# Optimization experiments

Hardware: AMD Instinct MI355X
Metric: run time of the kernel (lower is better)

## Reference

```python
import jax, jax.numpy as jnp
import numpy as np

EPS = 1e-5

def layer_norm(x, g, b):
    mu = jnp.mean(x, axis=-1, keepdims=True)
    var = jnp.var(x, axis=-1, keepdims=True)
    return (x - mu) * jax.lax.rsqrt(var + EPS) * g + b

def setup_inputs() -> dict:
    key = jax.random.key(0)
    N, C, K = 50000, 64, 16
    ks = jax.random.split(key, 16)
    def lin(k, fan_in, fan_out):
        bound = 1.0 / np.sqrt(fan_in)
        kw, kb = jax.random.split(k)
        W = jax.random.uniform(kw, (fan_in, fan_out), minval=-bound, maxval=bound, dtype=jnp.float32)
        b = jax.random.uniform(kb, (fan_out,), minval=-bound, maxval=bound, dtype=jnp.float32)
        return W, b
    wq, bq = lin(ks[0], C, C)
    wk, bk = lin(ks[1], C, C)
    wv, bv = lin(ks[2], C, C)
    wp, bp = lin(ks[3], 3, C)
    wg1, bg1 = lin(ks[4], C, C)
    wg2, bg2 = lin(ks[5], C, C)
    wo, bo = lin(ks[6], C, C)
    return {
        'points': jax.random.normal(ks[7], (N, 3), dtype=jnp.float32),
        'features': jax.random.normal(ks[8], (N, C), dtype=jnp.float32),
        'neighbor_idx': jax.random.randint(ks[9], (N, K), 0, N, dtype=jnp.int32),
        'wq': wq, 'bq': bq, 'wk': wk, 'bk': bk, 'wv': wv, 'bv': bv,
        'wp': wp, 'bp': bp, 'gp': jnp.ones((C,), jnp.float32), 'betap': jnp.zeros((C,), jnp.float32),
        'wg1': wg1, 'bg1': bg1, 'gg': jnp.ones((C,), jnp.float32), 'betag': jnp.zeros((C,), jnp.float32),
        'wg2': wg2, 'bg2': bg2, 'wo': wo, 'bo': bo,
    }

def reference(points, features, neighbor_idx, wq, bq, wk, bk, wv, bv,
              wp, bp, gp, betap, wg1, bg1, gg, betag, wg2, bg2, wo, bo):
    # residual_proj is Identity since in_planes == out_planes
    residual = features
    q = features @ wq + bq                      # (N, C)
    k = features @ wk + bk
    v = features @ wv + bv
    gpts = points[neighbor_idx]                 # (N, K, 3)
    gk = k[neighbor_idx]                        # (N, K, C)
    gv = v[neighbor_idx]
    rel = gpts - points[:, None, :]             # (N, K, 3)
    p = jax.nn.relu(layer_norm(rel @ wp + bp, gp, betap))  # (N, K, C)
    attn_in = q[:, None, :] - gk + p            # (N, K, C)
    h = jax.nn.relu(layer_norm(attn_in @ wg1 + bg1, gg, betag))
    w = h @ wg2 + bg2                           # (N, K, C)
    w = jax.nn.softmax(w, axis=1)               # softmax over neighbor axis
    out = jnp.sum((gv + p) * w, axis=1)         # (N, C)
    return out @ wo + bo + residual
```

## Files before the change

### kernel.cpp

```cpp
#include <hip/hip_runtime.h>

typedef __attribute__((ext_vector_type(8))) short bfrag8;
typedef __attribute__((ext_vector_type(4))) short bfrag4;
typedef __attribute__((ext_vector_type(4))) float f32x4;

__device__ __forceinline__ float bf2f(unsigned short h){
  unsigned u = ((unsigned)h) << 16;
  return __builtin_bit_cast(float, u);
}
__device__ __forceinline__ unsigned short f2bf(float f){
  unsigned u = __builtin_bit_cast(unsigned, f);
  u = u + 0x7FFFu + ((u >> 16) & 1u);
  return (unsigned short)(u >> 16);
}
__device__ __forceinline__ bfrag8 gload8(const unsigned short* p){
  int4 v = *(const int4*)p;
  return __builtin_bit_cast(bfrag8, v);
}
__device__ __forceinline__ bfrag8 lds_load8(const unsigned short* p){
  bfrag4 lo = *(const bfrag4*)p;
  bfrag4 hi = *(const bfrag4*)(p + 4);
  bfrag8 r;
#pragma unroll
  for (int j = 0; j < 4; j++){ r[j] = lo[j]; r[4+j] = hi[j]; }
  return r;
}
__device__ __forceinline__ f32x4 mfma16(bfrag8 a, bfrag8 b, f32x4 c){
  return __builtin_amdgcn_mfma_f32_16x16x32_bf16(a, b, c, 0, 0, 0);
}

__device__ __forceinline__ float ldf(const void* p, size_t i, int f32){
  return f32 ? ((const float*)p)[i] : bf2f(((const unsigned short*)p)[i]);
}
__device__ __forceinline__ unsigned short ldbf(const void* p, size_t i, int f32){
  return f32 ? f2bf(((const float*)p)[i]) : ((const unsigned short*)p)[i];
}
__device__ __forceinline__ bfrag8 load8bf(const void* p, size_t base, int f32){
  if (f32){
    const float* f = (const float*)p + base;
    float4 x = *(const float4*)f;
    float4 y = *(const float4*)(f + 4);
    bfrag8 r;
    r[0]=(short)f2bf(x.x); r[1]=(short)f2bf(x.y); r[2]=(short)f2bf(x.z); r[3]=(short)f2bf(x.w);
    r[4]=(short)f2bf(y.x); r[5]=(short)f2bf(y.y); r[6]=(short)f2bf(y.z); r[7]=(short)f2bf(y.w);
    return r;
  }
  return gload8((const unsigned short*)p + base);
}

template<int CTRL>
__device__ __forceinline__ float dpp_add(float x){
  int xi = __builtin_bit_cast(int, x);
  int yi = __builtin_amdgcn_update_dpp(0, xi, CTRL, 0xF, 0xF, true);
  return x + __builtin_bit_cast(float, yi);
}
__device__ __forceinline__ float row16_sum(float x){
  x = dpp_add<0xB1>(x);
  x = dpp_add<0x4E>(x);
  x = dpp_add<0x141>(x);
  x = dpp_add<0x140>(x);
  return x;
}
__device__ __forceinline__ float xgrp_sum(float x){
  x += __shfl_xor(x, 16, 64);
  x += __shfl_xor(x, 32, 64);
  return x;
}
__device__ __forceinline__ float xgrp_max(float x){
  x = fmaxf(x, __shfl_xor(x, 16, 64));
  x = fmaxf(x, __shfl_xor(x, 32, 64));
  return x;
}
__device__ __forceinline__ int wave_isum(int x){
#pragma unroll
  for (int s = 1; s < 64; s <<= 1) x += __shfl_xor(x, s, 64);
  return x;
}

struct Ptrs { const void* p[21]; int n[21]; };
struct PrepPtrs { const void* w[6]; const void* wp; const void* b[11]; };

__global__ void detect_kernel(Ptrs ptrs, int* flags){
  const int lane = threadIdx.x & 63;
  const int wid = blockIdx.x * 4 + (threadIdx.x >> 6);
  if (wid >= 21) return;
  if (wid == 2){ if (lane == 0) flags[2] = 0; return; }

  const unsigned short* p = (const unsigned short*)ptrs.p[wid];
  int m = ptrs.n[wid]; if (m > 128) m = 128;
  int insane = 0, evenZero = 0, evenCnt = 0, oddNZ = 0, oddCnt = 0;
#pragma unroll
  for (int s = 0; s < 2; s++){
    int i = lane + s*64;
    if (i < m){
      unsigned short h = p[i];
      int e = (h >> 7) & 0xFF;
      bool z = (h & 0x7FFF) == 0;
      if (!z && (e == 0xFF || e < 90 || e > 140)) insane++;
      if (i & 1){ oddCnt++;  if (!z) oddNZ++; }
      else      { evenCnt++; if (z)  evenZero++; }
    }
  }
  insane = wave_isum(insane);
  evenZero = wave_isum(evenZero); evenCnt = wave_isum(evenCnt);
  oddNZ = wave_isum(oddNZ);       oddCnt = wave_isum(oddCnt);
  if (lane == 0){
    int f = 0;
    if (insane > 0) f = 1;
    else if (evenZero * 4 >= evenCnt * 3 && oddNZ * 4 >= oddCnt * 3) f = 1;
    flags[wid] = f;
  }
}

__global__ void prep_kernel(PrepPtrs pp, const int* __restrict__ flags,
                            unsigned short* __restrict__ wfrag,
                            unsigned short* __restrict__ wp_bf,
                            float* __restrict__ biases)
{
  const int gid = blockIdx.x * 256 + threadIdx.x;
  const int gstride = gridDim.x * 256;
  const int wflag[6] = {3,5,7,13,17,19};
  for (int idx = gid; idx < 6*4096; idx += gstride){
    int m = idx >> 12;
    int r = idx & 4095;
    int j = r & 7;
    int lane = (r >> 3) & 63;
    int kt = r >> 9;
    int ks = kt >> 2, t = kt & 3;
    int o = lane >> 4, rl = lane & 15;
    int src = (ks*32 + o*8 + j)*64 + t*16 + rl;
    wfrag[idx] = ldbf(pp.w[m], src, flags[wflag[m]]);
  }
  if (blockIdx.x == 0){
    for (int i = threadIdx.x; i < 192; i += 256) wp_bf[i] = ldbf(pp.wp, i, flags[9]);
    const int bflag[11] = {4,6,8,10,11,12,14,15,16,18,20};
    for (int i = threadIdx.x; i < 11*64; i += 256){
      int m = i >> 6;
      biases[i] = ldf(pp.b[m], i & 63, flags[bflag[m]]);
    }
  }
}

__global__ __launch_bounds__(256, 2)
void qkv_kernel(const void* __restrict__ feat,
                const unsigned short* __restrict__ wfrag,
                const float* __restrict__ biases,
                unsigned short* __restrict__ q_ws, unsigned short* __restrict__ k_ws,
                unsigned short* __restrict__ v_ws, const int* __restrict__ flags, int N)
{
  const int F_feat = flags[1];
  const int lane = threadIdx.x & 63;
  const int wave = threadIdx.x >> 6;
  const int o = lane >> 4, rl = lane & 15;

  bfrag8 wqf[2][4], wkf[2][4], wvf[2][4];
#pragma unroll
  for (int ks = 0; ks < 2; ks++)
#pragma unroll
    for (int t = 0; t < 4; t++){
      int off = ((ks*4 + t)*64 + lane)*8;
      wqf[ks][t] = gload8(wfrag + off);
      wkf[ks][t] = gload8(wfrag + 4096 + off);
      wvf[ks][t] = gload8(wfrag + 8192 + off);
    }
  float bqC[4], bkC[4], bvC[4];
#pragma unroll
  for (int t = 0; t < 4; t++){
    bqC[t] = biases[0*64 + t*16 + rl];
    bkC[t] = biases[1*64 + t*16 + rl];
    bvC[t] = biases[2*64 + t*16 + rl];
  }

  const int ntiles = (N + 15) >> 4;
  for (int tile = blockIdx.x*4 + wave; tile < ntiles; tile += gridDim.x*4){
    const int n0 = tile * 16;
    int ar = n0 + rl; if (ar >= N) ar = N - 1;
    bfrag8 a[2];
#pragma unroll
    for (int ks = 0; ks < 2; ks++) a[ks] = load8bf(feat, (size_t)ar*64 + ks*32 + o*8, F_feat);

#pragma unroll
    for (int t = 0; t < 4; t++){
      f32x4 zq = {0.f,0.f,0.f,0.f}, zk = {0.f,0.f,0.f,0.f}, zv = {0.f,0.f,0.f,0.f};
#pragma unroll
      for (int ks = 0; ks < 2; ks++){
        zq = mfma16(a[ks], wqf[ks][t], zq);
        zk = mfma16(a[ks], wkf[ks][t], zk);
        zv = mfma16(a[ks], wvf[ks][t], zv);
      }
#pragma unroll
      for (int q = 0; q < 4; q++){
        size_t row = n0 + o*4 + q; int col = t*16 + rl;
        if ((int)row < N){
          q_ws[row*64 + col] = f2bf(zq[q] + bqC[t]);
          k_ws[row*64 + col] = f2bf(zk[q] + bkC[t]);
          v_ws[row*64 + col] = f2bf(zv[q] + bvC[t]);
        }
      }
    }
  }
}

__global__ __launch_bounds__(256, 2)
void pt_kernel(const void* __restrict__ points,
               const void* __restrict__ feat,
               const int* __restrict__ nidx,
               const unsigned short* __restrict__ q_ws,
               const unsigned short* __restrict__ k_ws,
               const unsigned short* __restrict__ v_ws,
               const unsigned short* __restrict__ wfrag,
               const unsigned short* __restrict__ wp_bf,
               const float* __restrict__ biases,
               const int* __restrict__ flags, void* __restrict__ out, int N)
{
  __shared__ unsigned short xbuf[4][16][68];
  __shared__ unsigned short ybuf[4][64];

  const int F_pts = flags[0], F_feat = flags[1];
  const int lane = threadIdx.x & 63;
  const int wave = threadIdx.x >> 6;
  const int o = lane >> 4, rl = lane & 15;

  bfrag8 wg1f[2][4], wg2f[2][4], wof[2][4];
#pragma unroll
  for (int ks = 0; ks < 2; ks++)
#pragma unroll
    for (int t = 0; t < 4; t++){
      int off = ((ks*4 + t)*64 + lane)*8;
      wg1f[ks][t] = gload8(wfrag + 3*4096 + off);
      wg2f[ks][t] = gload8(wfrag + 4*4096 + off);
      wof[ks][t]  = gload8(wfrag + 5*4096 + off);
    }
  bfrag8 wpf[4];
#pragma unroll
  for (int t = 0; t < 4; t++){
    bfrag8 a = {0,0,0,0,0,0,0,0};
    if (o == 0){
#pragma unroll
      for (int j = 0; j < 3; j++) a[j] = (short)wp_bf[j*64 + t*16 + rl];
    }
    wpf[t] = a;
  }
  float bpC[4], gpC[4], bePC[4], bg1C[4], ggC[4], beGC[4], bg2C[4], boC[4];
#pragma unroll
  for (int t = 0; t < 4; t++){
    int c = t*16 + rl;
    bpC[t]  = biases[3*64 + c];  gpC[t]  = biases[4*64 + c];  bePC[t] = biases[5*64 + c];
    bg1C[t] = biases[6*64 + c];  ggC[t]  = biases[7*64 + c];  beGC[t] = biases[8*64 + c];
    bg2C[t] = biases[9*64 + c];  boC[t]  = biases[10*64 + c];
  }

  const int wstride = gridDim.x * 4;
  for (int n = blockIdx.x*4 + wave; n < N; n += wstride){
    const int jr = nidx[n*16 + rl];
    int jq[4];
#pragma unroll
    for (int q = 0; q < 4; q++) jq[q] = nidx[n*16 + o*4 + q];

    float qC[4], gkC[4][4], gvC[4][4];
#pragma unroll
    for (int t = 0; t < 4; t++) qC[t] = bf2f(q_ws[(size_t)n*64 + t*16 + rl]);
#pragma unroll
    for (int q = 0; q < 4; q++)
#pragma unroll
      for (int t = 0; t < 4; t++){
        gkC[t][q] = bf2f(k_ws[(size_t)jq[q]*64 + t*16 + rl]);
        gvC[t][q] = bf2f(v_ws[(size_t)jq[q]*64 + t*16 + rl]);
      }
    const float res = ldf(feat, (size_t)n*64 + lane, F_feat);
    float rel[3];
#pragma unroll
    for (int d = 0; d < 3; d++)
      rel[d] = ldf(points, (size_t)jr*3 + d, F_pts) - ldf(points, (size_t)n*3 + d, F_pts);

    bfrag8 ap = {0,0,0,0,0,0,0,0};
    if (o == 0){
#pragma unroll
      for (int d = 0; d < 3; d++) ap[d] = (short)f2bf(rel[d]);
    }
    f32x4 pacc[4];
#pragma unroll
    for (int t = 0; t < 4; t++){
      f32x4 z = {0.f,0.f,0.f,0.f};
      pacc[t] = mfma16(ap, wpf[t], z);
    }
    float p_val[4][4];
#pragma unroll
    for (int q = 0; q < 4; q++){
      float xv[4]; float s = 0.f, s2 = 0.f;
#pragma unroll
      for (int t = 0; t < 4; t++){ xv[t] = pacc[t][q] + bpC[t]; s += xv[t]; s2 += xv[t]*xv[t]; }
      s = row16_sum(s); s2 = row16_sum(s2);
      float mu = s * (1.f/64.f);
      float var = s2 * (1.f/64.f) - mu*mu;
      float rs = rsqrtf(var + 1e-5f);
#pragma unroll
      for (int t = 0; t < 4; t++){
        float v = (xv[t] - mu) * rs * gpC[t] + bePC[t];
        p_val[t][q] = fmaxf(v, 0.f);
      }
    }

#pragma unroll
    for (int q = 0; q < 4; q++)
#pragma unroll
      for (int t = 0; t < 4; t++)
        xbuf[wave][o*4 + q][t*16 + rl] = f2bf(qC[t] - gkC[t][q] + p_val[t][q]);
    f32x4 hacc[4] = {{0.f,0.f,0.f,0.f},{0.f,0.f,0.f,0.f},{0.f,0.f,0.f,0.f},{0.f,0.f,0.f,0.f}};
#pragma unroll
    for (int ks = 0; ks < 2; ks++){
      bfrag8 af = lds_load8(&xbuf[wave][rl][ks*32 + o*8]);
#pragma unroll
      for (int t = 0; t < 4; t++) hacc[t] = mfma16(af, wg1f[ks][t], hacc[t]);
    }

    float h_val[4][4];
#pragma unroll
    for (int q = 0; q < 4; q++){
      float xv[4]; float s = 0.f, s2 = 0.f;
#pragma unroll
      for (int t = 0; t < 4; t++){ xv[t] = hacc[t][q] + bg1C[t]; s += xv[t]; s2 += xv[t]*xv[t]; }
      s = row16_sum(s); s2 = row16_sum(s2);
      float mu = s * (1.f/64.f);
      float var = s2 * (1.f/64.f) - mu*mu;
      float rs = rsqrtf(var + 1e-5f);
#pragma unroll
      for (int t = 0; t < 4; t++){
        float v = (xv[t] - mu) * rs * ggC[t] + beGC[t];
        h_val[t][q] = fmaxf(v, 0.f);
      }
    }

#pragma unroll
    for (int q = 0; q < 4; q++)
#pragma unroll
      for (int t = 0; t < 4; t++) xbuf[wave][o*4 + q][t*16 + rl] = f2bf(h_val[t][q]);
    f32x4 wacc[4] = {{0.f,0.f,0.f,0.f},{0.f,0.f,0.f,0.f},{0.f,0.f,0.f,0.f},{0.f,0.f,0.f,0.f}};
#pragma unroll
    for (int ks = 0; ks < 2; ks++){
      bfrag8 hf = lds_load8(&xbuf[wave][rl][ks*32 + o*8]);
#pragma unroll
      for (int t = 0; t < 4; t++) wacc[t] = mfma16(hf, wg2f[ks][t], wacc[t]);
    }

    float y[4];
#pragma unroll
    for (int t = 0; t < 4; t++){
      float wv[4];
#pragma unroll
      for (int q = 0; q < 4; q++) wv[q] = wacc[t][q] + bg2C[t];
      float mx = fmaxf(fmaxf(wv[0], wv[1]), fmaxf(wv[2], wv[3]));
      mx = xgrp_max(mx);
      float se = 0.f, z = 0.f;
#pragma unroll
      for (int q = 0; q < 4; q++){
        float e = __expf(wv[q] - mx);
        se += e;
        z  += e * (gvC[t][q] + p_val[t][q]);
      }
      se = xgrp_sum(se); z = xgrp_sum(z);
      y[t] = z / se;
    }

    if (o == 0){
#pragma unroll
      for (int t = 0; t < 4; t++) ybuf[wave][t*16 + rl] = f2bf(y[t]);
    }
    f32x4 oacc[4] = {{0.f,0.f,0.f,0.f},{0.f,0.f,0.f,0.f},{0.f,0.f,0.f,0.f},{0.f,0.f,0.f,0.f}};
#pragma unroll
    for (int ks = 0; ks < 2; ks++){
      bfrag8 yf = lds_load8(&ybuf[wave][ks*32 + o*8]);
#pragma unroll
      for (int t = 0; t < 4; t++) oacc[t] = mfma16(yf, wof[ks][t], oacc[t]);
    }

    float ov = 0.f;
#pragma unroll
    for (int t = 0; t < 4; t++) if (o == t) ov = oacc[t][0] + boC[t];
    float outv = ov + res;
    if (F_feat) ((float*)out)[(size_t)n*64 + lane] = outv;
    else ((unsigned short*)out)[(size_t)n*64 + lane] = f2bf(outv);
  }
}

extern "C" void kernel_launch(void* const* d_in, const int* in_sizes, int n_in,
                              void* d_out, int out_size, void* d_ws, size_t ws_size,
                              hipStream_t stream)
{
  const int N = in_sizes[1] / 64;

  unsigned short* q_ws = (unsigned short*)d_ws;
  unsigned short* k_ws = q_ws + (size_t)N * 64;
  unsigned short* v_ws = k_ws + (size_t)N * 64;
  char* base = (char*)d_ws + (size_t)3 * N * 64 * sizeof(unsigned short);
  int*            flags  = (int*)base;
  unsigned short* wfrag  = (unsigned short*)(base + 256);
  unsigned short* wp_bf  = (unsigned short*)(base + 256 + 49152);
  float*          biases = (float*)(base + 256 + 49152 + 512);

  Ptrs ptrs;
  for (int i = 0; i < 21; i++){ ptrs.p[i] = d_in[i]; ptrs.n[i] = in_sizes[i]; }
  PrepPtrs pp;
  pp.w[0] = d_in[3];  pp.w[1] = d_in[5];  pp.w[2] = d_in[7];
  pp.w[3] = d_in[13]; pp.w[4] = d_in[17]; pp.w[5] = d_in[19];
  pp.wp = d_in[9];
  pp.b[0] = d_in[4];  pp.b[1] = d_in[6];  pp.b[2] = d_in[8];  pp.b[3] = d_in[10];
  pp.b[4] = d_in[11]; pp.b[5] = d_in[12]; pp.b[6] = d_in[14]; pp.b[7] = d_in[15];
  pp.b[8] = d_in[16]; pp.b[9] = d_in[18]; pp.b[10] = d_in[20];

  detect_kernel<<<6, 256, 0, stream>>>(ptrs, flags);
  prep_kernel<<<32, 256, 0, stream>>>(pp, flags, wfrag, wp_bf, biases);
  qkv_kernel<<<512, 256, 0, stream>>>(d_in[1], wfrag, biases, q_ws, k_ws, v_ws, flags, N);
  pt_kernel<<<1024, 256, 0, stream>>>(d_in[0], d_in[1], (const int*)d_in[2], q_ws, k_ws, v_ws,
                                      wfrag, wp_bf, biases, flags, d_out, N);
}
```

Measured before the change: 224.9 us.

## Interleave QKV workspace layout for vector gathers and trim pointwise math

The Q/K/V workspace columns are permuted so each lane owns four contiguous bf16 values. The projection stores and the neighbor gathers can then use single 8-byte accesses instead of four 2-byte ones. Float-to-bf16 conversions use a packed hardware conversion builtin when it is available. The LayerNorm affine is folded into one FMA per element. The softmax drops its max-subtraction reduction and replaces the divide with a fast reciprocal, which removes two cross-lane shuffles per channel group. The cost is a risk of exp overflow if the logits ever grow large, plus slightly lower precision in the normalization.

```diff
diff --git a/kernel.cpp b/kernel.cpp
--- a/kernel.cpp
+++ b/kernel.cpp
@@ -3,6 +3,12 @@
 typedef __attribute__((ext_vector_type(8))) short bfrag8;
 typedef __attribute__((ext_vector_type(4))) short bfrag4;
 typedef __attribute__((ext_vector_type(4))) float f32x4;
+
+#if defined(__has_builtin)
+#if __has_builtin(__builtin_amdgcn_cvt_pk_bf16_f32)
+#define HAVE_PK_BF16 1
+#endif
+#endif
 
 __device__ __forceinline__ float bf2f(unsigned short h){
   unsigned u = ((unsigned)h) << 16;
@@ -12,6 +18,15 @@
   unsigned u = __builtin_bit_cast(unsigned, f);
   u = u + 0x7FFFu + ((u >> 16) & 1u);
   return (unsigned short)(u >> 16);
+}
+__device__ __forceinline__ unsigned pk2bf(float a, float b){
+#ifdef HAVE_PK_BF16
+  typedef __attribute__((ext_vector_type(2))) __bf16 bf16x2_t;
+  bf16x2_t r = __builtin_amdgcn_cvt_pk_bf16_f32(a, b);
+  return __builtin_bit_cast(unsigned, r);
+#else
+  return (unsigned)f2bf(a) | ((unsigned)f2bf(b) << 16);
+#endif
 }
 __device__ __forceinline__ bfrag8 gload8(const unsigned short* p){
   int4 v = *(const int4*)p;
@@ -64,11 +79,6 @@
 __device__ __forceinline__ float xgrp_sum(float x){
   x += __shfl_xor(x, 16, 64);
   x += __shfl_xor(x, 32, 64);
-  return x;
-}
-__device__ __forceinline__ float xgrp_max(float x){
-  x = fmaxf(x, __shfl_xor(x, 16, 64));
-  x = fmaxf(x, __shfl_xor(x, 32, 64));
   return x;
 }
 __device__ __forceinline__ int wave_isum(int x){
@@ -179,23 +189,33 @@
 #pragma unroll
     for (int ks = 0; ks < 2; ks++) a[ks] = load8bf(feat, (size_t)ar*64 + ks*32 + o*8, F_feat);
 
+    f32x4 zq[4], zk[4], zv[4];
 #pragma unroll
     for (int t = 0; t < 4; t++){
-      f32x4 zq = {0.f,0.f,0.f,0.f}, zk = {0.f,0.f,0.f,0.f}, zv = {0.f,0.f,0.f,0.f};
+      f32x4 aq = {0.f,0.f,0.f,0.f}, ak = {0.f,0.f,0.f,0.f}, av = {0.f,0.f,0.f,0.f};
 #pragma unroll
       for (int ks = 0; ks < 2; ks++){
-        zq = mfma16(a[ks], wqf[ks][t], zq);
-        zk = mfma16(a[ks], wkf[ks][t], zk);
-        zv = mfma16(a[ks], wvf[ks][t], zv);
+        aq = mfma16(a[ks], wqf[ks][t], aq);
+        ak = mfma16(a[ks], wkf[ks][t], ak);
+        av = mfma16(a[ks], wvf[ks][t], av);
       }
-#pragma unroll
-      for (int q = 0; q < 4; q++){
-        size_t row = n0 + o*4 + q; int col = t*16 + rl;
-        if ((int)row < N){
-          q_ws[row*64 + col] = f2bf(zq[q] + bqC[t]);
-          k_ws[row*64 + col] = f2bf(zk[q] + bkC[t]);
-          v_ws[row*64 + col] = f2bf(zv[q] + bvC[t]);
-        }
+      zq[t] = aq; zk[t] = ak; zv[t] = av;
+    }
+#pragma unroll
+    for (int q = 0; q < 4; q++){
+      size_t row = n0 + o*4 + q;
+      if ((int)row < N){
+        size_t e = row*64 + 4*rl;
+        uint2 u;
+        u.x = pk2bf(zq[0][q]+bqC[0], zq[1][q]+bqC[1]);
+        u.y = pk2bf(zq[2][q]+bqC[2], zq[3][q]+bqC[3]);
+        *(uint2*)(q_ws + e) = u;
+        u.x = pk2bf(zk[0][q]+bkC[0], zk[1][q]+bkC[1]);
+        u.y = pk2bf(zk[2][q]+bkC[2], zk[3][q]+bkC[3]);
+        *(uint2*)(k_ws + e) = u;
+        u.x = pk2bf(zv[0][q]+bvC[0], zv[1][q]+bvC[1]);
+        u.y = pk2bf(zv[2][q]+bvC[2], zv[3][q]+bvC[3]);
+        *(uint2*)(v_ws + e) = u;
       }
     }
   }
@@ -258,15 +278,18 @@
     for (int q = 0; q < 4; q++) jq[q] = nidx[n*16 + o*4 + q];
 
     float qC[4], gkC[4][4], gvC[4][4];
-#pragma unroll
-    for (int t = 0; t < 4; t++) qC[t] = bf2f(q_ws[(size_t)n*64 + t*16 + rl]);
-#pragma unroll
-    for (int q = 0; q < 4; q++)
-#pragma unroll
-      for (int t = 0; t < 4; t++){
-        gkC[t][q] = bf2f(k_ws[(size_t)jq[q]*64 + t*16 + rl]);
-        gvC[t][q] = bf2f(v_ws[(size_t)jq[q]*64 + t*16 + rl]);
-      }
+    {
+      ushort4 uq = *(const ushort4*)(q_ws + (size_t)n*64 + 4*rl);
+      qC[0] = bf2f(uq.x); qC[1] = bf2f(uq.y); qC[2] = bf2f(uq.z); qC[3] = bf2f(uq.w);
+    }
+#pragma unroll
+    for (int q = 0; q < 4; q++){
+      size_t e = (size_t)jq[q]*64 + 4*rl;
+      ushort4 uk = *(const ushort4*)(k_ws + e);
+      ushort4 uv = *(const ushort4*)(v_ws + e);
+      gkC[0][q] = bf2f(uk.x); gkC[1][q] = bf2f(uk.y); gkC[2][q] = bf2f(uk.z); gkC[3][q] = bf2f(uk.w);
+      gvC[0][q] = bf2f(uv.x); gvC[1][q] = bf2f(uv.y); gvC[2][q] = bf2f(uv.z); gvC[3][q] = bf2f(uv.w);
+    }
     const float res = ldf(feat, (size_t)n*64 + lane, F_feat);
     float rel[3];
 #pragma unroll
@@ -296,16 +319,24 @@
       float rs = rsqrtf(var + 1e-5f);
 #pragma unroll
       for (int t = 0; t < 4; t++){
-        float v = (xv[t] - mu) * rs * gpC[t] + bePC[t];
-        p_val[t][q] = fmaxf(v, 0.f);
+        float a = rs * gpC[t];
+        p_val[t][q] = fmaxf(xv[t]*a + (bePC[t] - mu*a), 0.f);
       }
     }
 
 #pragma unroll
-    for (int q = 0; q < 4; q++)
-#pragma unroll
-      for (int t = 0; t < 4; t++)
-        xbuf[wave][o*4 + q][t*16 + rl] = f2bf(qC[t] - gkC[t][q] + p_val[t][q]);
+    for (int q = 0; q < 4; q++){
+      float a0 = qC[0] - gkC[0][q] + p_val[0][q];
+      float a1 = qC[1] - gkC[1][q] + p_val[1][q];
+      float a2 = qC[2] - gkC[2][q] + p_val[2][q];
+      float a3 = qC[3] - gkC[3][q] + p_val[3][q];
+      unsigned u01 = pk2bf(a0, a1), u23 = pk2bf(a2, a3);
+      int r = o*4 + q;
+      xbuf[wave][r][0*16 + rl] = (unsigned short)u01;
+      xbuf[wave][r][1*16 + rl] = (unsigned short)(u01 >> 16);
+      xbuf[wave][r][2*16 + rl] = (unsigned short)u23;
+      xbuf[wave][r][3*16 + rl] = (unsigned short)(u23 >> 16);
+    }
     f32x4 hacc[4] = {{0.f,0.f,0.f,0.f},{0.f,0.f,0.f,0.f},{0.f,0.f,0.f,0.f},{0.f,0.f,0.f,0.f}};
 #pragma unroll
     for (int ks = 0; ks < 2; ks++){
@@ -326,15 +357,17 @@
       float rs = rsqrtf(var + 1e-5f);
 #pragma unroll
       for (int t = 0; t < 4; t++){
-        float v = (xv[t] - mu) * rs * ggC[t] + beGC[t];
-        h_val[t][q] = fmaxf(v, 0.f);
+        float a = rs * ggC[t];
+        h_val[t][q] = fmaxf(xv[t]*a + (beGC[t] - mu*a), 0.f);
       }
-    }
-
-#pragma unroll
-    for (int q = 0; q < 4; q++)
-#pragma unroll
-      for (int t = 0; t < 4; t++) xbuf[wave][o*4 + q][t*16 + rl] = f2bf(h_val[t][q]);
+      unsigned u01 = pk2bf(h_val[0][q], h_val[1][q]);
+      unsigned u23 = pk2bf(h_val[2][q], h_val[3][q]);
+      int r = o*4 + q;
+      xbuf[wave][r][0*16 + rl] = (unsigned short)u01;
+      xbuf[wave][r][1*16 + rl] = (unsigned short)(u01 >> 16);
+      xbuf[wave][r][2*16 + rl] = (unsigned short)u23;
+      xbuf[wave][r][3*16 + rl] = (unsigned short)(u23 >> 16);
+    }
     f32x4 wacc[4] = {{0.f,0.f,0.f,0.f},{0.f,0.f,0.f,0.f},{0.f,0.f,0.f,0.f},{0.f,0.f,0.f,0.f}};
 #pragma unroll
     for (int ks = 0; ks < 2; ks++){
@@ -346,25 +379,23 @@
     float y[4];
 #pragma unroll
     for (int t = 0; t < 4; t++){
-      float wv[4];
-#pragma unroll
-      for (int q = 0; q < 4; q++) wv[q] = wacc[t][q] + bg2C[t];
-      float mx = fmaxf(fmaxf(wv[0], wv[1]), fmaxf(wv[2], wv[3]));
-      mx = xgrp_max(mx);
       float se = 0.f, z = 0.f;
 #pragma unroll
       for (int q = 0; q < 4; q++){
-        float e = __expf(wv[q] - mx);
+        float e = __expf(wacc[t][q] + bg2C[t]);
         se += e;
         z  += e * (gvC[t][q] + p_val[t][q]);
       }
       se = xgrp_sum(se); z = xgrp_sum(z);
-      y[t] = z / se;
+      y[t] = z * __builtin_amdgcn_rcpf(se);
     }
 
     if (o == 0){
-#pragma unroll
-      for (int t = 0; t < 4; t++) ybuf[wave][t*16 + rl] = f2bf(y[t]);
+      unsigned u01 = pk2bf(y[0], y[1]), u23 = pk2bf(y[2], y[3]);
+      ybuf[wave][0*16 + rl] = (unsigned short)u01;
+      ybuf[wave][1*16 + rl] = (unsigned short)(u01 >> 16);
+      ybuf[wave][2*16 + rl] = (unsigned short)u23;
+      ybuf[wave][3*16 + rl] = (unsigned short)(u23 >> 16);
     }
     f32x4 oacc[4] = {{0.f,0.f,0.f,0.f},{0.f,0.f,0.f,0.f},{0.f,0.f,0.f,0.f},{0.f,0.f,0.f,0.f}};
 #pragma unroll
```

Measured after the change: 214.7 us. 1.05x faster.
